# Performance work log

Measured on AMD Instinct MI355X. Metric: run time of the kernel, lower is better.

## Reference

```python
import jax, jax.numpy as jnp
import numpy as np

N = 50000   # query points
N2 = 50000  # key/value points
C = 128     # n_channels
G = 8       # n_groups
S = 16      # n_samples
CS = C // G # n_share_channels
EPS = 1e-5


def setup_inputs() -> dict:
    key = jax.random.key(0)
    ks = jax.random.split(key, 16)
    std = 0.02
    return {
        "p": jax.random.normal(ks[0], (N, 3), jnp.float32),
        "x": jax.random.normal(ks[1], (N, C), jnp.float32),
        "p2": jax.random.normal(ks[2], (N2, 3), jnp.float32),
        "x2": jax.random.normal(ks[3], (N2, C), jnp.float32),
        "idx": jax.random.randint(ks[4], (N, S), 0, N2, jnp.int32),
        "Wq": jax.random.normal(ks[5], (C, C), jnp.float32) * std,
        "bq": jnp.zeros((C,), jnp.float32),
        "Wk": jax.random.normal(ks[6], (C, C), jnp.float32) * std,
        "bk": jnp.zeros((C,), jnp.float32),
        "Wv": jax.random.normal(ks[7], (C, C), jnp.float32) * std,
        "bv": jnp.zeros((C,), jnp.float32),
        # linear_p: Conv1d(3,3,1) -> BN(3) -> ReLU -> Conv1d(3, 2G, 1)
        "W1": jax.random.normal(ks[8], (3, 3), jnp.float32) * 0.5,
        "b1": jnp.zeros((3,), jnp.float32),
        "bn_gamma": jnp.ones((3,), jnp.float32),
        "bn_beta": jnp.zeros((3,), jnp.float32),
        "bn_mean": jnp.zeros((3,), jnp.float32),
        "bn_var": jnp.ones((3,), jnp.float32),
        "W2": jax.random.normal(ks[9], (2 * G, 3), jnp.float32) * 0.5,
        "b2": jnp.zeros((2 * G,), jnp.float32),
    }


def reference(p, x, p2, x2, idx,
              Wq, bq, Wk, bk, Wv, bv,
              W1, b1, bn_gamma, bn_beta, bn_mean, bn_var, W2, b2):
    n = x.shape[0]
    # Q/K/V projections
    x_q = x @ Wq.T + bq                       # (n, C)
    x_k = (x2 @ Wk.T + bk)[idx]               # (n, S, C)  KNN gather
    x_v = (x2 @ Wv.T + bv)[idx]               # (n, S, C)
    # relative positions
    p_r = p2[idx] - p[:, None, :]             # (n, S, 3)
    # linear_p (pointwise convs == per-neighbor MLP over the 3 coord channels)
    h = p_r @ W1.T + b1
    h = (h - bn_mean) * jax.lax.rsqrt(bn_var + EPS) * bn_gamma + bn_beta
    h = jax.nn.relu(h)
    pe = h @ W2.T + b2                        # (n, S, 2G)
    p_rq, p_rk = jnp.split(pe, 2, axis=-1)    # each (n, S, G)
    # grouped attention
    k4 = x_k.reshape(n, S, G, CS) + p_rk[..., None]
    q4 = x_q.reshape(n, 1, G, CS) + p_rq[..., None]
    logits = jnp.sum(k4 * q4, axis=-1) / np.float32(np.sqrt(CS))  # (n, S, G)
    w = jax.nn.softmax(logits, axis=1)        # softmax over neighbors
    out = jnp.einsum('nsgc,nsg->ngc', x_v.reshape(n, S, G, CS), w)
    return out.reshape(n, C)
```

## Files before the change

### kernel.cpp

```cpp
#include <hip/hip_runtime.h>
#include <hip/hip_bf16.h>

#define NQ   50000
#define NKV  50000
#define CC   128
#define GG   8
#define SS   16
#define CSH  16

typedef short    bf16x8 __attribute__((ext_vector_type(8)));
typedef float    f32x4  __attribute__((ext_vector_type(4)));
typedef unsigned u32x4  __attribute__((ext_vector_type(4)));
typedef unsigned u32x2  __attribute__((ext_vector_type(2)));
typedef int      i32x4  __attribute__((ext_vector_type(4)));

__device__ __forceinline__ float bf_lo(unsigned u){ union{unsigned x; float f;} v; v.x = u << 16;        return v.f; }
__device__ __forceinline__ float bf_hi(unsigned u){ union{unsigned x; float f;} v; v.x = u & 0xffff0000u; return v.f; }
__device__ __forceinline__ unsigned short f2bfu(float f){
    __hip_bfloat16 h = __float2bfloat16(f);
    return *reinterpret_cast<unsigned short*>(&h);
}
__device__ __forceinline__ short f2bfs(float f){
    __hip_bfloat16 h = __float2bfloat16(f);
    return *reinterpret_cast<short*>(&h);
}

__device__ __forceinline__ void load16bf(const __hip_bfloat16* ptr, float* o){
    const u32x4* p4 = reinterpret_cast<const u32x4*>(ptr);
    u32x4 a = p4[0]; u32x4 b = p4[1];
    o[0]=bf_lo(a[0]);  o[1]=bf_hi(a[0]);  o[2]=bf_lo(a[1]);  o[3]=bf_hi(a[1]);
    o[4]=bf_lo(a[2]);  o[5]=bf_hi(a[2]);  o[6]=bf_lo(a[3]);  o[7]=bf_hi(a[3]);
    o[8]=bf_lo(b[0]);  o[9]=bf_hi(b[0]);  o[10]=bf_lo(b[1]); o[11]=bf_hi(b[1]);
    o[12]=bf_lo(b[2]); o[13]=bf_hi(b[2]); o[14]=bf_lo(b[3]); o[15]=bf_hi(b[3]);
}

__device__ __forceinline__ bf16x8 cvt8(const float* p){
    const f32x4* q = reinterpret_cast<const f32x4*>(p);
    f32x4 u = q[0], v = q[1];
    bf16x8 r;
    r[0]=f2bfs(u[0]); r[1]=f2bfs(u[1]); r[2]=f2bfs(u[2]); r[3]=f2bfs(u[3]);
    r[4]=f2bfs(v[0]); r[5]=f2bfs(v[1]); r[6]=f2bfs(v[2]); r[7]=f2bfs(v[3]);
    return r;
}

__global__ __launch_bounds__(256) void qkv_gemm(
    const float* __restrict__ x,
    const float* __restrict__ x2,
    const float* __restrict__ Wq, const float* __restrict__ Wk,
    const float* __restrict__ Wv,
    const float* __restrict__ bq, const float* __restrict__ bk,
    const float* __restrict__ bv,
    __hip_bfloat16* __restrict__ Qf,
    __hip_bfloat16* __restrict__ KVf)
{
    __shared__ short lds16[16384];

    const int tid  = threadIdx.x;
    const int wave = tid >> 6;
    const int lane = tid & 63;
    const int r    = lane & 15;
    const int kq   = lane >> 4;
    const int base = blockIdx.x * 128 + wave * 32;
    const int proj = blockIdx.y;

    const float* src  = (proj == 0) ? x  : x2;
    const float* W    = (proj == 0) ? Wq : (proj == 1 ? Wk : Wv);
    const float* bias = (proj == 0) ? bq : (proj == 1 ? bk : bv);
    short* dstb   = (proj == 0) ? (short*)Qf : (short*)KVf;
    const int dstride = (proj == 0) ? CC : 2 * CC;
    const int hoff    = (proj == 2) ? CC : 0;

    bf16x8 bfrag[2][4];
    #pragma unroll
    for (int mt = 0; mt < 2; ++mt) {
        int row = base + mt * 16 + r;
        if (row >= NQ) row = NQ - 1;
        const float* xr = src + (size_t)row * CC + kq * 8;
        #pragma unroll
        for (int kb = 0; kb < 4; ++kb)
            bfrag[mt][kb] = cvt8(xr + kb * 32);
    }

    #pragma unroll
    for (int i = 0; i < 8; ++i) {
        const int o   = i * 2048 + tid * 8;
        const bf16x8 v = cvt8(W + o);
        const int row = o >> 7, col = o & 127;
        const int lchunk = (((row >> 4) * 4 + (col >> 5)) << 6)
                         + (((col >> 3) & 3) << 4) + (row & 15);
        *reinterpret_cast<bf16x8*>(&lds16[lchunk * 8]) = v;
    }
    __syncthreads();

    #pragma unroll
    for (int t = 0; t < 8; ++t) {
        bf16x8 af[4];
        #pragma unroll
        for (int kb = 0; kb < 4; ++kb)
            af[kb] = *reinterpret_cast<const bf16x8*>(
                &lds16[(((t * 4 + kb) << 6) + lane) * 8]);

        f32x4 acc0 = {0.f,0.f,0.f,0.f}, acc1 = {0.f,0.f,0.f,0.f};
        #pragma unroll
        for (int kb = 0; kb < 4; ++kb) {
            acc0 = __builtin_amdgcn_mfma_f32_16x16x32_bf16(af[kb], bfrag[0][kb], acc0, 0, 0, 0);
            acc1 = __builtin_amdgcn_mfma_f32_16x16x32_bf16(af[kb], bfrag[1][kb], acc1, 0, 0, 0);
        }

        const f32x4 bi = *reinterpret_cast<const f32x4*>(bias + t * 16 + kq * 4);
        #pragma unroll
        for (int mt = 0; mt < 2; ++mt) {
            const int row = base + mt * 16 + r;
            if (row < NQ) {
                const f32x4 a = mt ? acc1 : acc0;
                u32x2 pk;
                pk[0] = (unsigned)f2bfu(a[0] + bi[0]) | ((unsigned)f2bfu(a[1] + bi[1]) << 16);
                pk[1] = (unsigned)f2bfu(a[2] + bi[2]) | ((unsigned)f2bfu(a[3] + bi[3]) << 16);
                *reinterpret_cast<u32x2*>(
                    dstb + (size_t)row * dstride + hoff + t * 16 + kq * 4) = pk;
            }
        }
    }
}

__global__ __launch_bounds__(256) void attn_kernel(
    const float* __restrict__ p,
    const float* __restrict__ p2,
    const int*   __restrict__ idx,
    const float* __restrict__ W1,
    const float* __restrict__ b1,
    const float* __restrict__ bn_gamma,
    const float* __restrict__ bn_beta,
    const float* __restrict__ bn_mean,
    const float* __restrict__ bn_var,
    const float* __restrict__ W2,
    const float* __restrict__ b2,
    const __hip_bfloat16* __restrict__ Qf,
    const __hip_bfloat16* __restrict__ KVf,
    float* __restrict__ out)
{
    const int tid = blockIdx.x * 256 + threadIdx.x;
    const int n = tid >> 4;
    const int g = (tid >> 1) & 7;
    const int h = tid & 1;

    float fw1[3][3], fb1[3];
    #pragma unroll
    for (int j = 0; j < 3; ++j) {
        const float sc = bn_gamma[j] * rsqrtf(bn_var[j] + 1e-5f);
        #pragma unroll
        for (int k = 0; k < 3; ++k) fw1[j][k] = W1[j*3 + k] * sc;
        fb1[j] = (b1[j] - bn_mean[j]) * sc + bn_beta[j];
    }
    const float w2q0 = W2[g*3+0],     w2q1 = W2[g*3+1],     w2q2 = W2[g*3+2];
    const float w2k0 = W2[(g+8)*3+0], w2k1 = W2[(g+8)*3+1], w2k2 = W2[(g+8)*3+2];
    const float b2q = b2[g], b2k = b2[g+8];

    const float px = p[(size_t)n*3+0];
    const float py = p[(size_t)n*3+1];
    const float pz = p[(size_t)n*3+2];

    int nbr[8];
    {
        const i32x4* ip = reinterpret_cast<const i32x4*>(idx + (size_t)n * SS + h * 8);
        i32x4 i0 = ip[0], i1 = ip[1];
        nbr[0]=i0[0]; nbr[1]=i0[1]; nbr[2]=i0[2]; nbr[3]=i0[3];
        nbr[4]=i1[0]; nbr[5]=i1[1]; nbr[6]=i1[2]; nbr[7]=i1[3];
    }

    float q[CSH];
    load16bf(Qf + (size_t)n * CC + g * CSH, q);
    float sumq = 0.f;
    #pragma unroll
    for (int c = 0; c < CSH; ++c) sumq += q[c];

    float acc[CSH];
    #pragma unroll
    for (int c = 0; c < CSH; ++c) acc[c] = 0.f;
    float sum = 0.f;
    float m = -3.0e38f;

    #pragma unroll 4
    for (int s = 0; s < 8; ++s) {
        const int i = nbr[s];
        const __hip_bfloat16* kv = KVf + (size_t)i * (2 * CC) + g * CSH;

        float kk[CSH], vv[CSH];
        load16bf(kv, kk);
        load16bf(kv + CC, vv);

        const float rx = p2[(size_t)i*3+0] - px;
        const float ry = p2[(size_t)i*3+1] - py;
        const float rz = p2[(size_t)i*3+2] - pz;
        const float h0 = fmaxf(fw1[0][0]*rx + fw1[0][1]*ry + fw1[0][2]*rz + fb1[0], 0.f);
        const float h1 = fmaxf(fw1[1][0]*rx + fw1[1][1]*ry + fw1[1][2]*rz + fb1[1], 0.f);
        const float h2 = fmaxf(fw1[2][0]*rx + fw1[2][1]*ry + fw1[2][2]*rz + fb1[2], 0.f);
        const float prq = w2q0*h0 + w2q1*h1 + w2q2*h2 + b2q;
        const float prk = w2k0*h0 + w2k1*h1 + w2k2*h2 + b2k;

        float dot = 0.f, sumk = 0.f;
        #pragma unroll
        for (int c = 0; c < CSH; ++c) { dot += kk[c]*q[c]; sumk += kk[c]; }
        const float d = (dot + prq*sumk + prk*sumq + 16.f*prk*prq) * 0.25f;

        const float mnew = fmaxf(m, d);
        const float corr = __expf(m - mnew);
        const float w    = __expf(d - mnew);
        sum = sum * corr + w;
        #pragma unroll
        for (int c = 0; c < CSH; ++c) acc[c] = acc[c] * corr + w * vv[c];
        m = mnew;
    }

    const float mo = __shfl_xor(m, 1);
    const float M  = fmaxf(m, mo);
    const float cs = __expf(m  - M);
    const float co = __expf(mo - M);
    const float so = __shfl_xor(sum, 1);
    const float inv = 1.f / (sum * cs + so * co);
    const float mycs = cs * inv, pco = co * inv;

    float o[8];
    #pragma unroll
    for (int j = 0; j < 8; ++j) {
        const float send = h ? acc[j] : acc[j + 8];
        const float recv = __shfl_xor(send, 1);
        const float own  = h ? acc[j + 8] : acc[j];
        o[j] = own * mycs + recv * pco;
    }

    f32x4* op = reinterpret_cast<f32x4*>(out + (size_t)n * CC + g * CSH + h * 8);
    f32x4 o0 = {o[0], o[1], o[2], o[3]};
    f32x4 o1 = {o[4], o[5], o[6], o[7]};
    op[0] = o0; op[1] = o1;
}

extern "C" void kernel_launch(void* const* d_in, const int* in_sizes, int n_in,
                              void* d_out, int out_size, void* d_ws, size_t ws_size,
                              hipStream_t stream) {
    const float* p   = (const float*)d_in[0];
    const float* x   = (const float*)d_in[1];
    const float* p2  = (const float*)d_in[2];
    const float* x2  = (const float*)d_in[3];
    const int*   idx = (const int*)d_in[4];
    const float* Wq  = (const float*)d_in[5];
    const float* bq  = (const float*)d_in[6];
    const float* Wk  = (const float*)d_in[7];
    const float* bk  = (const float*)d_in[8];
    const float* Wv  = (const float*)d_in[9];
    const float* bv  = (const float*)d_in[10];
    const float* W1  = (const float*)d_in[11];
    const float* b1  = (const float*)d_in[12];
    const float* bng = (const float*)d_in[13];
    const float* bnb = (const float*)d_in[14];
    const float* bnm = (const float*)d_in[15];
    const float* bnv = (const float*)d_in[16];
    const float* W2  = (const float*)d_in[17];
    const float* b2  = (const float*)d_in[18];
    float* out = (float*)d_out;

    __hip_bfloat16* Qf  = (__hip_bfloat16*)d_ws;
    __hip_bfloat16* KVf = Qf + (size_t)NQ * CC;

    qkv_gemm<<<dim3(391, 3), 256, 0, stream>>>(
        x, x2, Wq, Wk, Wv, bq, bk, bv, Qf, KVf);

    attn_kernel<<<3125, 256, 0, stream>>>(
        p, p2, idx, W1, b1, bng, bnb, bnm, bnv, W2, b2, Qf, KVf, out);
}
```

Baseline: 208.6 us.

## Assign one thread per query-group and software-pipeline neighbor gathers

The attention kernel now gives each thread a whole (query, group) pair and all 16 neighbors, instead of splitting neighbors across two threads that merged results through shuffles. It adds a two-deep software prefetch of the K/V rows and neighbor positions so that gathers overlap with the online-softmax math. It also keeps q and V in packed bf16 registers and converts them on the fly. This halves thread count and removes the cross-lane merge, but each thread does more serial work with fewer waves in flight to hide gather latency. The last iterations issue redundant prefetches of the final neighbor.

```diff
diff --git a/kernel.cpp b/kernel.cpp
--- a/kernel.cpp
+++ b/kernel.cpp
@@ -25,13 +25,22 @@
     return *reinterpret_cast<short*>(&h);
 }
 
-__device__ __forceinline__ void load16bf(const __hip_bfloat16* ptr, float* o){
-    const u32x4* p4 = reinterpret_cast<const u32x4*>(ptr);
-    u32x4 a = p4[0]; u32x4 b = p4[1];
-    o[0]=bf_lo(a[0]);  o[1]=bf_hi(a[0]);  o[2]=bf_lo(a[1]);  o[3]=bf_hi(a[1]);
-    o[4]=bf_lo(a[2]);  o[5]=bf_hi(a[2]);  o[6]=bf_lo(a[3]);  o[7]=bf_hi(a[3]);
-    o[8]=bf_lo(b[0]);  o[9]=bf_hi(b[0]);  o[10]=bf_lo(b[1]); o[11]=bf_hi(b[1]);
-    o[12]=bf_lo(b[2]); o[13]=bf_hi(b[2]); o[14]=bf_lo(b[3]); o[15]=bf_hi(b[3]);
+__device__ __forceinline__ float dot8_qraw(const u32x4& k, const u32x4& qr, float& sumk){
+    float d = 0.f;
+    #pragma unroll
+    for (int j = 0; j < 4; ++j) {
+        const float klo = bf_lo(k[j]), khi = bf_hi(k[j]);
+        d    += klo * bf_lo(qr[j]) + khi * bf_hi(qr[j]);
+        sumk += klo + khi;
+    }
+    return d;
+}
+__device__ __forceinline__ void acc8_lazy(const u32x4& a, float corr, float w, float* acc8){
+    #pragma unroll
+    for (int j = 0; j < 4; ++j) {
+        acc8[2*j]   = acc8[2*j]  * corr + w * bf_lo(a[j]);
+        acc8[2*j+1] = acc8[2*j+1]* corr + w * bf_hi(a[j]);
+    }
 }
 
 __device__ __forceinline__ bf16x8 cvt8(const float* p){
@@ -140,9 +149,9 @@
     float* __restrict__ out)
 {
     const int tid = blockIdx.x * 256 + threadIdx.x;
-    const int n = tid >> 4;
-    const int g = (tid >> 1) & 7;
-    const int h = tid & 1;
+    if (tid >= NQ * GG) return;
+    const int n = tid >> 3;
+    const int g = tid & 7;
 
     float fw1[3][3], fb1[3];
     #pragma unroll
@@ -160,19 +169,32 @@
     const float py = p[(size_t)n*3+1];
     const float pz = p[(size_t)n*3+2];
 
-    int nbr[8];
+    const int* __restrict__ idxr = idx + (size_t)n * SS;
+
+    u32x4 qr0, qr1;
     {
-        const i32x4* ip = reinterpret_cast<const i32x4*>(idx + (size_t)n * SS + h * 8);
-        i32x4 i0 = ip[0], i1 = ip[1];
-        nbr[0]=i0[0]; nbr[1]=i0[1]; nbr[2]=i0[2]; nbr[3]=i0[3];
-        nbr[4]=i1[0]; nbr[5]=i1[1]; nbr[6]=i1[2]; nbr[7]=i1[3];
-    }
-
-    float q[CSH];
-    load16bf(Qf + (size_t)n * CC + g * CSH, q);
+        const u32x4* qp = reinterpret_cast<const u32x4*>(Qf + (size_t)n * CC + g * CSH);
+        qr0 = qp[0]; qr1 = qp[1];
+    }
     float sumq = 0.f;
     #pragma unroll
-    for (int c = 0; c < CSH; ++c) sumq += q[c];
+    for (int j = 0; j < 4; ++j) sumq += bf_lo(qr0[j]) + bf_hi(qr0[j])
+                                      + bf_lo(qr1[j]) + bf_hi(qr1[j]);
+
+    u32x4 kA0, kA1, vA0, vA1; float rAx, rAy, rAz;
+    u32x4 kB0, kB1, vB0, vB1; float rBx, rBy, rBz;
+
+    auto PF = [&](int s, u32x4& k0, u32x4& k1, u32x4& v0, u32x4& v1,
+                  float& rx, float& ry, float& rz) {
+        const int i = idxr[s];
+        const u32x4* kv = reinterpret_cast<const u32x4*>(
+            KVf + (size_t)i * (2 * CC) + g * CSH);
+        k0 = kv[0]; k1 = kv[1];
+        v0 = kv[16]; v1 = kv[17];
+        rx = p2[(size_t)i*3+0] - px;
+        ry = p2[(size_t)i*3+1] - py;
+        rz = p2[(size_t)i*3+2] - pz;
+    };
 
     float acc[CSH];
     #pragma unroll
@@ -180,59 +202,49 @@
     float sum = 0.f;
     float m = -3.0e38f;
 
-    #pragma unroll 4
-    for (int s = 0; s < 8; ++s) {
-        const int i = nbr[s];
-        const __hip_bfloat16* kv = KVf + (size_t)i * (2 * CC) + g * CSH;
-
-        float kk[CSH], vv[CSH];
-        load16bf(kv, kk);
-        load16bf(kv + CC, vv);
-
-        const float rx = p2[(size_t)i*3+0] - px;
-        const float ry = p2[(size_t)i*3+1] - py;
-        const float rz = p2[(size_t)i*3+2] - pz;
+    auto CONSUME = [&](const u32x4& k0, const u32x4& k1,
+                       const u32x4& v0, const u32x4& v1,
+                       float rx, float ry, float rz) {
         const float h0 = fmaxf(fw1[0][0]*rx + fw1[0][1]*ry + fw1[0][2]*rz + fb1[0], 0.f);
         const float h1 = fmaxf(fw1[1][0]*rx + fw1[1][1]*ry + fw1[1][2]*rz + fb1[1], 0.f);
         const float h2 = fmaxf(fw1[2][0]*rx + fw1[2][1]*ry + fw1[2][2]*rz + fb1[2], 0.f);
         const float prq = w2q0*h0 + w2q1*h1 + w2q2*h2 + b2q;
         const float prk = w2k0*h0 + w2k1*h1 + w2k2*h2 + b2k;
 
-        float dot = 0.f, sumk = 0.f;
-        #pragma unroll
-        for (int c = 0; c < CSH; ++c) { dot += kk[c]*q[c]; sumk += kk[c]; }
+        float sumk = 0.f;
+        const float dot = dot8_qraw(k0, qr0, sumk) + dot8_qraw(k1, qr1, sumk);
         const float d = (dot + prq*sumk + prk*sumq + 16.f*prk*prq) * 0.25f;
 
         const float mnew = fmaxf(m, d);
         const float corr = __expf(m - mnew);
         const float w    = __expf(d - mnew);
         sum = sum * corr + w;
-        #pragma unroll
-        for (int c = 0; c < CSH; ++c) acc[c] = acc[c] * corr + w * vv[c];
+        acc8_lazy(v0, corr, w, acc);
+        acc8_lazy(v1, corr, w, acc + 8);
         m = mnew;
-    }
-
-    const float mo = __shfl_xor(m, 1);
-    const float M  = fmaxf(m, mo);
-    const float cs = __expf(m  - M);
-    const float co = __expf(mo - M);
-    const float so = __shfl_xor(sum, 1);
-    const float inv = 1.f / (sum * cs + so * co);
-    const float mycs = cs * inv, pco = co * inv;
-
-    float o[8];
-    #pragma unroll
-    for (int j = 0; j < 8; ++j) {
-        const float send = h ? acc[j] : acc[j + 8];
-        const float recv = __shfl_xor(send, 1);
-        const float own  = h ? acc[j + 8] : acc[j];
-        o[j] = own * mycs + recv * pco;
-    }
-
-    f32x4* op = reinterpret_cast<f32x4*>(out + (size_t)n * CC + g * CSH + h * 8);
-    f32x4 o0 = {o[0], o[1], o[2], o[3]};
-    f32x4 o1 = {o[4], o[5], o[6], o[7]};
-    op[0] = o0; op[1] = o1;
+    };
+
+    PF(0, kA0, kA1, vA0, vA1, rAx, rAy, rAz);
+    PF(1, kB0, kB1, vB0, vB1, rBx, rBy, rBz);
+
+    #pragma unroll 1
+    for (int it = 0; it < 8; ++it) {
+        const int sA = (2*it + 2 < SS) ? (2*it + 2) : (SS - 1);
+        const int sB = (2*it + 3 < SS) ? (2*it + 3) : (SS - 1);
+        CONSUME(kA0, kA1, vA0, vA1, rAx, rAy, rAz);
+        PF(sA, kA0, kA1, vA0, vA1, rAx, rAy, rAz);
+        CONSUME(kB0, kB1, vB0, vB1, rBx, rBy, rBz);
+        PF(sB, kB0, kB1, vB0, vB1, rBx, rBy, rBz);
+    }
+
+    const float inv = 1.f / sum;
+
+    f32x4* op = reinterpret_cast<f32x4*>(out + (size_t)n * CC + g * CSH);
+    f32x4 o0 = {acc[0]*inv,  acc[1]*inv,  acc[2]*inv,  acc[3]*inv};
+    f32x4 o1 = {acc[4]*inv,  acc[5]*inv,  acc[6]*inv,  acc[7]*inv};
+    f32x4 o2 = {acc[8]*inv,  acc[9]*inv,  acc[10]*inv, acc[11]*inv};
+    f32x4 o3 = {acc[12]*inv, acc[13]*inv, acc[14]*inv, acc[15]*inv};
+    op[0] = o0; op[1] = o1; op[2] = o2; op[3] = o3;
 }
 
 extern "C" void kernel_launch(void* const* d_in, const int* in_sizes, int n_in,
@@ -265,6 +277,6 @@
     qkv_gemm<<<dim3(391, 3), 256, 0, stream>>>(
         x, x2, Wq, Wk, Wv, bq, bk, bv, Qf, KVf);
 
-    attn_kernel<<<3125, 256, 0, stream>>>(
+    attn_kernel<<<(NQ * GG + 255) / 256, 256, 0, stream>>>(
         p, p2, idx, W1, b1, bng, bnb, bnm, bnv, W2, b2, Qf, KVf, out);
 }
```

After: 211.1 us. No clear change (+1.2%).
